# Optimization experiments

Measured on AMD Instinct MI355X. Metric: run time of the kernel, lower is better.

The kernel has to match this reference:

```python
import jax, jax.numpy as jnp
import numpy as np

LN_EPS = 1e-5
B, T, H = 32, 1024, 1024


def _layer_norm(v, g, b):
    m = v.mean(-1, keepdims=True)
    var = ((v - m) ** 2).mean(-1, keepdims=True)
    return (v - m) / jnp.sqrt(var + LN_EPS) * g + b


def setup_inputs() -> dict:
    key = jax.random.key(0)
    ks = jax.random.split(key, 10)
    s_t = 1.0 / np.sqrt(T)
    s_h = 1.0 / np.sqrt(H)
    return {
        "x": jax.random.normal(ks[0], (B, T, H), jnp.float32),
        # temporal MLP (square T x T, triangular-masked), torch Linear layout [out, in]
        "tw1": jax.random.uniform(ks[1], (T, T), jnp.float32, -s_t, s_t),
        "tb1": jax.random.uniform(ks[2], (T,), jnp.float32, -s_t, s_t),
        "tw2": jax.random.uniform(ks[3], (T, T), jnp.float32, -s_t, s_t),
        "tb2": jax.random.uniform(ks[4], (T,), jnp.float32, -s_t, s_t),
        # channel MLP (square H x H)
        "cw1": jax.random.uniform(ks[5], (H, H), jnp.float32, -s_h, s_h),
        "cb1": jax.random.uniform(ks[6], (H,), jnp.float32, -s_h, s_h),
        "cw2": jax.random.uniform(ks[7], (H, H), jnp.float32, -s_h, s_h),
        "cb2": jax.random.uniform(ks[8], (H,), jnp.float32, -s_h, s_h),
        # LayerNorm affine params
        "ln1_g": jnp.ones((H,), jnp.float32),
        "ln1_b": jnp.zeros((H,), jnp.float32),
        "ln2_g": jnp.ones((H,), jnp.float32),
        "ln2_b": jnp.zeros((H,), jnp.float32),
    }


def reference(x, tw1, tb1, tw2, tb2, cw1, cb1, cw2, cb2, ln1_g, ln1_b, ln2_g, ln2_b):
    t = tw1.shape[0]
    mask = jnp.tril(jnp.ones((t, t), x.dtype))  # diagonal=0: include self
    # temporal mixing: LN -> swap -> masked Linear -> GELU -> masked Linear -> swap
    y = _layer_norm(x, ln1_g, ln1_b)
    y = jnp.swapaxes(y, 1, 2)  # [B, H, T]
    y = y @ (mask * tw1).T + tb1
    y = jax.nn.gelu(y, approximate=False)
    y = y @ (mask * tw2).T + tb2
    y = jnp.swapaxes(y, 1, 2)  # [B, T, H]
    x = x + y
    # channel mixing: LN -> Linear -> GELU -> Linear
    y2 = _layer_norm(x, ln2_g, ln2_b)
    y2 = jax.nn.gelu(y2 @ cw1.T + cb1, approximate=False) @ cw2.T + cb2
    return x + y2
```

## Files before the change

kernel.cpp:

```cpp
#include <hip/hip_runtime.h>
#include <hip/hip_bf16.h>

#define BDIM 32
#define TDIM 1024
#define HDIM 1024
#define AS1 __attribute__((address_space(1)))
#define AS3 __attribute__((address_space(3)))

typedef __attribute__((ext_vector_type(8))) short short8;
typedef __attribute__((ext_vector_type(8))) unsigned short ushort8;
typedef __attribute__((ext_vector_type(4))) unsigned short u16x4;
typedef __attribute__((ext_vector_type(4))) float f32x4;

__device__ __forceinline__ float b2f(unsigned short h){ return __uint_as_float(((unsigned)h)<<16); }
__device__ __forceinline__ unsigned short f2b(float f){
  unsigned u = __float_as_uint(f);
  u += 0x7fffu + ((u>>16)&1u);
  return (unsigned short)(u>>16);
}
__device__ __forceinline__ float gelu_f(float v){ return 0.5f*v*(1.0f+erff(v*0.70710678118f)); }
__device__ __forceinline__ void stv(float* p, float v){ *p = v; }
__device__ __forceinline__ void stv(unsigned short* p, float v){ *p = f2b(v); }
__device__ __forceinline__ float ldr(float v){ return v; }
__device__ __forceinline__ float ldr(unsigned short v){ return b2f(v); }

__global__ void prep_weights(const float* __restrict__ w1, const float* __restrict__ w2,
                             const float* __restrict__ c1, const float* __restrict__ c2,
                             unsigned short* __restrict__ w1m, unsigned short* __restrict__ w2m,
                             unsigned short* __restrict__ c1b, unsigned short* __restrict__ c2b){
  int idx = blockIdx.x*blockDim.x + threadIdx.x;
  int e = idx*4;
  int i = e >> 10, j0 = e & 1023;
  f32x4 a = *(const f32x4*)(w1+e);
  f32x4 b = *(const f32x4*)(w2+e);
  f32x4 c = *(const f32x4*)(c1+e);
  f32x4 d = *(const f32x4*)(c2+e);
  u16x4 av, bv, cv, dv;
  #pragma unroll
  for (int q=0;q<4;++q){
    float am = (j0+q <= i) ? a[q] : 0.f;
    float bm = (j0+q <= i) ? b[q] : 0.f;
    av[q]=f2b(am); bv[q]=f2b(bm); cv[q]=f2b(c[q]); dv[q]=f2b(d[q]);
  }
  *(u16x4*)(w1m+e)=av; *(u16x4*)(w2m+e)=bv; *(u16x4*)(c1b+e)=cv; *(u16x4*)(c2b+e)=dv;
}

__global__ void ln_stats(const float* __restrict__ p, float* __restrict__ mean,
                         float* __restrict__ rstd){
  int wid = threadIdx.x>>6, lane = threadIdx.x&63;
  int row = blockIdx.x*4 + wid;
  const float* pr = p + (size_t)row*HDIM;
  float s=0.f, s2=0.f;
  #pragma unroll
  for (int it=0; it<4; ++it){
    f32x4 v = *(const f32x4*)(pr + it*256 + lane*4);
    #pragma unroll
    for (int c=0;c<4;++c){ s += v[c]; s2 += v[c]*v[c]; }
  }
  #pragma unroll
  for (int off=32; off>0; off>>=1){ s += __shfl_xor(s,off,64); s2 += __shfl_xor(s2,off,64); }
  if (lane==0){
    float m = s * (1.0f/HDIM);
    float var = s2 * (1.0f/HDIM) - m*m;
    mean[row]=m; rstd[row]=rsqrtf(var + 1e-5f);
  }
}

__global__ void ln_norm_transpose(const float* __restrict__ x, const float* __restrict__ mean,
                                  const float* __restrict__ rstd, const float* __restrict__ g,
                                  const float* __restrict__ bta, unsigned short* __restrict__ xnT){
  __shared__ float tile[64][65];
  int t0 = blockIdx.x*64, h0 = blockIdx.y*64, b = blockIdx.z;
  int tid = threadIdx.x;
  int rr = tid>>3, c8 = tid&7;
  size_t base = (size_t)b*TDIM*HDIM;
  #pragma unroll
  for (int p=0;p<2;++p){
    int r = rr + p*32;
    int trow = t0 + r;
    float m = mean[b*TDIM + trow], rs = rstd[b*TDIM + trow];
    f32x4 v0 = *(const f32x4*)(x + base + (size_t)trow*HDIM + h0 + c8*8);
    f32x4 v1 = *(const f32x4*)(x + base + (size_t)trow*HDIM + h0 + c8*8 + 4);
    #pragma unroll
    for (int c=0;c<4;++c){
      int h = c8*8+c;
      tile[r][h]   = (v0[c]-m)*rs*g[h0+h]   + bta[h0+h];
      tile[r][h+4] = (v1[c]-m)*rs*g[h0+h+4] + bta[h0+h+4];
    }
  }
  __syncthreads();
  #pragma unroll
  for (int p=0;p<2;++p){
    int hr = rr + p*32;
    ushort8 ov;
    #pragma unroll
    for (int c=0;c<8;++c) ov[c] = f2b(tile[c8*8+c][hr]);
    *(ushort8*)(xnT + base + (size_t)(h0+hr)*TDIM + t0 + c8*8) = ov;
  }
}

__global__ void ln_fused(const unsigned short* __restrict__ p, const float* __restrict__ g,
                         const float* __restrict__ bta, unsigned short* __restrict__ o){
  int wid = threadIdx.x>>6, lane = threadIdx.x&63;
  size_t row = (size_t)blockIdx.x*4 + wid;
  const unsigned short* pr = p + row*HDIM + lane*16;
  ushort8 v0 = *(const ushort8*)(pr);
  ushort8 v1 = *(const ushort8*)(pr+8);
  float f[16];
  float s=0.f, s2=0.f;
  #pragma unroll
  for (int c=0;c<8;++c){ f[c]=b2f(v0[c]); f[c+8]=b2f(v1[c]); }
  #pragma unroll
  for (int c=0;c<16;++c){ s += f[c]; s2 += f[c]*f[c]; }
  #pragma unroll
  for (int off=32; off>0; off>>=1){ s += __shfl_xor(s,off,64); s2 += __shfl_xor(s2,off,64); }
  float m = s * (1.0f/HDIM);
  float rs = rsqrtf(s2*(1.0f/HDIM) - m*m + 1e-5f);
  int h0 = lane*16;
  ushort8 o0, o1;
  #pragma unroll
  for (int c=0;c<8;++c){
    o0[c] = f2b((f[c]-m)*rs*g[h0+c] + bta[h0+c]);
    o1[c] = f2b((f[c+8]-m)*rs*g[h0+c+8] + bta[h0+c+8]);
  }
  *(ushort8*)(o + row*HDIM + h0) = o0;
  *(ushort8*)(o + row*HDIM + h0 + 8) = o1;
}

#define GATE(N) asm volatile("s_waitcnt vmcnt(" #N ")" ::: "memory")
#define BAR()   __builtin_amdgcn_s_barrier()

template<int MODE, typename CT, typename RT>
__global__ __launch_bounds__(512,1)
void gemmq(const unsigned short* __restrict__ act, const unsigned short* __restrict__ wgt,
           CT* __restrict__ C, const float* __restrict__ bias, const RT* __restrict__ resid){
  extern __shared__ char LDS[];
  const int bid = blockIdx.x;
  const int tile = (bid & 7)*64 + (bid >> 3);
  const int panel = tile >> 2;
  int inner = tile & 3;
  if constexpr (MODE==1 || MODE==2){ if (bid & 256) inner ^= 3; }
  const unsigned short *pa, *pb;
  size_t cbase; int rg0, cg0, kend;
  if constexpr (MODE==1){
    int b = panel>>2, mt = panel&3;
    pa = act + (size_t)b*1048576 + (size_t)mt*262144;
    pb = wgt + (size_t)inner*262144;
    kend = (inner+1)*256;
    cbase = (size_t)b*1048576; rg0 = mt*256; cg0 = inner*256;
  } else if constexpr (MODE==2){
    int b = panel>>2, nt = panel&3;
    pa = wgt + (size_t)inner*262144;
    pb = act + (size_t)b*1048576 + (size_t)nt*262144;
    kend = (inner+1)*256;
    cbase = (size_t)b*1048576; rg0 = inner*256; cg0 = nt*256;
  } else {
    pa = act + (size_t)panel*262144;
    pb = wgt + (size_t)inner*262144;
    kend = 1024;
    cbase = 0; rg0 = panel*256; cg0 = inner*256;
  }
  const int tid = threadIdx.x, lane = tid&63, wid = tid>>6;
  const int wrow = (wid>>2)*64;
  const int wcol = (wid&3)*32;
  const int l15 = lane&15, l4b = (lane>>4)<<4;
  f32x4 acc[8][4];
  #pragma unroll
  for (int i=0;i<8;++i)
    #pragma unroll
    for (int j=0;j<4;++j) acc[i][j] = (f32x4)(0.f);

  const int NT = kend>>6;

  auto STAGE = [&](int dstbuf, int half, int st){
    const unsigned short* src = (half<2) ? pa : pb;
    const int rbase = (half&1)<<7;
    char* dst = LDS + (dstbuf<<16) + (half<<14);
    const int k0 = st<<6;
    #pragma unroll
    for (int l=0;l<2;++l){
      int W = tid*16 + (l<<13);
      int r = W>>7;
      int cs = (W&127) ^ ((r&7)<<4);
      __builtin_amdgcn_global_load_lds(
        (const AS1 void*)(src + (size_t)(rbase+r)*1024 + k0 + (cs>>1)),
        (AS3 void*)(dst + W), 16, 0, 0);
    }
  };

  auto LDA = [&](int buf, int qa, int i, int s)->short8{
    int ra = wrow + i*16 + l15;
    int L = (ra<<7) + (((s<<6) + l4b) ^ ((ra&7)<<4));
    return *(const short8*)(LDS + (buf<<16) + (qa<<14) + L);
  };
  auto LDB = [&](int buf, int qb, int j, int s)->short8{
    int rb = wcol + j*16 + l15;
    int L = (rb<<7) + (((s<<6) + l4b) ^ ((rb&7)<<4));
    return *(const short8*)(LDS + (buf<<16) + ((2+qb)<<14) + L);
  };

  short8 aR[2][4], bR[2][2];

#define MFMAQ(qa,qb)                                                         \
  __builtin_amdgcn_s_setprio(1);                                             \
  _Pragma("unroll") for (int s=0;s<2;++s)                                    \
    _Pragma("unroll") for (int i=0;i<4;++i)                                  \
      _Pragma("unroll") for (int j=0;j<2;++j)                                \
        acc[(qa)*4+i][(qb)*2+j] = __builtin_amdgcn_mfma_f32_16x16x32_bf16(   \
            aR[s][i], bR[s][j], acc[(qa)*4+i][(qb)*2+j], 0,0,0);             \
  __builtin_amdgcn_s_setprio(0);

#define TILE_BODY(BUF, TT)                                                   \
  {                                                                          \
    const int nsrc = ((TT)+1 < NT) ? (TT)+1 : (TT);                          \
    STAGE(BUF^1, 0, nsrc); STAGE(BUF^1, 2, nsrc);                            \
    STAGE(BUF^1, 1, nsrc); STAGE(BUF^1, 3, nsrc);                            \
    GATE(8); BAR();                                                          \
    _Pragma("unroll") for (int s=0;s<2;++s){                                 \
      _Pragma("unroll") for (int i=0;i<4;++i) aR[s][i] = LDA(BUF,0,i,s);     \
      _Pragma("unroll") for (int j=0;j<2;++j) bR[s][j] = LDB(BUF,0,j,s);     \
    }                                                                        \
    MFMAQ(0,0)                                                               \
    _Pragma("unroll") for (int s=0;s<2;++s)                                  \
      _Pragma("unroll") for (int j=0;j<2;++j) bR[s][j] = LDB(BUF,1,j,s);     \
    MFMAQ(0,1)                                                               \
    _Pragma("unroll") for (int s=0;s<2;++s)                                  \
      _Pragma("unroll") for (int i=0;i<4;++i) aR[s][i] = LDA(BUF,1,i,s);     \
    MFMAQ(1,1)                                                               \
    _Pragma("unroll") for (int s=0;s<2;++s)                                  \
      _Pragma("unroll") for (int j=0;j<2;++j) bR[s][j] = LDB(BUF,0,j,s);     \
    MFMAQ(1,0)                                                               \
    BAR();                                                                   \
  }

  STAGE(0,0,0); STAGE(0,2,0); STAGE(0,1,0); STAGE(0,3,0);
  GATE(0); BAR();

  for (int t=0; t<NT; t+=2){
    TILE_BODY(0, t)
    TILE_BODY(1, t+1)
  }
#undef TILE_BODY
#undef MFMAQ

  GATE(0);

  #pragma unroll
  for (int I=0;I<8;++I){
    int rbase = rg0 + (I>>2)*128 + wrow + (I&3)*16 + ((lane>>4)<<2);
    #pragma unroll
    for (int J=0;J<4;++J){
      int cg = cg0 + (J>>1)*128 + wcol + (J&1)*16 + l15;
      float bn = (MODE!=2) ? bias[cg] : 0.f;
      #pragma unroll
      for (int r=0;r<4;++r){
        int rg = rbase + r;
        float v = acc[I][J][r];
        if (MODE==1 || MODE==3){ v += bn; v = gelu_f(v); }
        else if (MODE==2){ v += bias[rg]; v += ldr(resid[cbase + (size_t)rg*1024 + cg]); }
        else { v += bn; v += ldr(resid[cbase + (size_t)rg*1024 + cg]); }
        stv(&C[cbase + (size_t)rg*1024 + cg], v);
      }
    }
  }
}

extern "C" void kernel_launch(void* const* d_in, const int* in_sizes, int n_in,
                              void* d_out, int out_size, void* d_ws, size_t ws_size,
                              hipStream_t stream){
  const float* x    = (const float*)d_in[0];
  const float* tw1  = (const float*)d_in[1];
  const float* tb1  = (const float*)d_in[2];
  const float* tw2  = (const float*)d_in[3];
  const float* tb2  = (const float*)d_in[4];
  const float* cw1  = (const float*)d_in[5];
  const float* cb1  = (const float*)d_in[6];
  const float* cw2  = (const float*)d_in[7];
  const float* cb2  = (const float*)d_in[8];
  const float* g1   = (const float*)d_in[9];
  const float* bb1  = (const float*)d_in[10];
  const float* g2   = (const float*)d_in[11];
  const float* bb2  = (const float*)d_in[12];
  float* out = (float*)d_out;

  char* ws = (char*)d_ws;
  unsigned short* bufA = (unsigned short*)(ws);
  unsigned short* bufB = (unsigned short*)(ws + 67108864);
  unsigned short* xmid = (unsigned short*)(ws + 134217728);
  unsigned short* w1m  = (unsigned short*)(ws + 201326592);
  unsigned short* w2m  = (unsigned short*)(ws + 203423744);
  unsigned short* c1b  = (unsigned short*)(ws + 205520896);
  unsigned short* c2b  = (unsigned short*)(ws + 207618048);
  float* meanb = (float*)(ws + 209715200);
  float* rstdb = (float*)(ws + 209846272);

  prep_weights<<<1024,256,0,stream>>>(tw1,tw2,cw1,cw2,w1m,w2m,c1b,c2b);
  ln_stats<<<8192,256,0,stream>>>(x, meanb, rstdb);
  ln_norm_transpose<<<dim3(16,16,32),256,0,stream>>>(x, meanb, rstdb, g1, bb1, bufA);
  gemmq<1,unsigned short,float><<<512,512,131072,stream>>>(bufA, w1m, bufB, tb1, (const float*)nullptr);
  gemmq<2,unsigned short,float><<<512,512,131072,stream>>>(bufB, w2m, xmid, tb2, x);
  ln_fused<<<8192,256,0,stream>>>(xmid, g2, bb2, bufA);
  gemmq<3,unsigned short,unsigned short><<<512,512,131072,stream>>>(bufA, c1b, bufB, cb1, (const unsigned short*)nullptr);
  gemmq<4,float,unsigned short><<<512,512,131072,stream>>>(bufB, c2b, out, cb2, xmid);
}
```

Measured before the change: 501.4 us.

## Use 16 waves per GEMM block with 64x64 per-wave subtiles

The bf16 MFMA GEMM block grows from 512 to 1024 threads, so each of 16 waves computes a 64x64 sub-tile of the 256x256 output with 16 accumulators instead of 32. Each thread now issues one LDS-async load per staged half instead of two, and the quadrant-ordered MFMA schedule becomes a simple per-k-slice loop over B fragments. The aim is more waves to hide latency and lower register pressure per wave. The cost is more waves contending for barriers and LDS bandwidth, plus loss of the hand-tuned A/B fragment reuse ordering.

```diff
diff --git a/kernel.cpp b/kernel.cpp
--- a/kernel.cpp
+++ b/kernel.cpp
@@ -131,8 +131,8 @@
 #define BAR()   __builtin_amdgcn_s_barrier()
 
 template<int MODE, typename CT, typename RT>
-__global__ __launch_bounds__(512,1)
-void gemmq(const unsigned short* __restrict__ act, const unsigned short* __restrict__ wgt,
+__global__ __launch_bounds__(1024,1)
+void gemmw(const unsigned short* __restrict__ act, const unsigned short* __restrict__ wgt,
            CT* __restrict__ C, const float* __restrict__ bias, const RT* __restrict__ resid){
   extern __shared__ char LDS[];
   const int bid = blockIdx.x;
@@ -162,11 +162,14 @@
   }
   const int tid = threadIdx.x, lane = tid&63, wid = tid>>6;
   const int wrow = (wid>>2)*64;
-  const int wcol = (wid&3)*32;
+  const int wcol = (wid&3)*64;
   const int l15 = lane&15, l4b = (lane>>4)<<4;
-  f32x4 acc[8][4];
-  #pragma unroll
-  for (int i=0;i<8;++i)
+  const int abase = (wrow>>7)<<14;
+  const int bbase = 32768 + ((wcol>>7)<<14);
+  const int arow0 = wrow & 127, brow0 = wcol & 127;
+  f32x4 acc[4][4];
+  #pragma unroll
+  for (int i=0;i<4;++i)
     #pragma unroll
     for (int j=0;j<4;++j) acc[i][j] = (f32x4)(0.f);
 
@@ -176,64 +179,47 @@
     const unsigned short* src = (half<2) ? pa : pb;
     const int rbase = (half&1)<<7;
     char* dst = LDS + (dstbuf<<16) + (half<<14);
-    const int k0 = st<<6;
-    #pragma unroll
-    for (int l=0;l<2;++l){
-      int W = tid*16 + (l<<13);
-      int r = W>>7;
-      int cs = (W&127) ^ ((r&7)<<4);
-      __builtin_amdgcn_global_load_lds(
-        (const AS1 void*)(src + (size_t)(rbase+r)*1024 + k0 + (cs>>1)),
-        (AS3 void*)(dst + W), 16, 0, 0);
-    }
+    int W = tid*16;
+    int r = W>>7;
+    int cs = (W&127) ^ ((r&7)<<4);
+    __builtin_amdgcn_global_load_lds(
+      (const AS1 void*)(src + (size_t)(rbase+r)*1024 + (st<<6) + (cs>>1)),
+      (AS3 void*)(dst + W), 16, 0, 0);
   };
 
-  auto LDA = [&](int buf, int qa, int i, int s)->short8{
-    int ra = wrow + i*16 + l15;
+  auto LDA = [&](int buf, int i, int s)->short8{
+    int ra = arow0 + i*16 + l15;
     int L = (ra<<7) + (((s<<6) + l4b) ^ ((ra&7)<<4));
-    return *(const short8*)(LDS + (buf<<16) + (qa<<14) + L);
+    return *(const short8*)(LDS + (buf<<16) + abase + L);
   };
-  auto LDB = [&](int buf, int qb, int j, int s)->short8{
-    int rb = wcol + j*16 + l15;
+  auto LDB = [&](int buf, int j, int s)->short8{
+    int rb = brow0 + j*16 + l15;
     int L = (rb<<7) + (((s<<6) + l4b) ^ ((rb&7)<<4));
-    return *(const short8*)(LDS + (buf<<16) + ((2+qb)<<14) + L);
+    return *(const short8*)(LDS + (buf<<16) + bbase + L);
   };
-
-  short8 aR[2][4], bR[2][2];
-
-#define MFMAQ(qa,qb)                                                         \
-  __builtin_amdgcn_s_setprio(1);                                             \
-  _Pragma("unroll") for (int s=0;s<2;++s)                                    \
-    _Pragma("unroll") for (int i=0;i<4;++i)                                  \
-      _Pragma("unroll") for (int j=0;j<2;++j)                                \
-        acc[(qa)*4+i][(qb)*2+j] = __builtin_amdgcn_mfma_f32_16x16x32_bf16(   \
-            aR[s][i], bR[s][j], acc[(qa)*4+i][(qb)*2+j], 0,0,0);             \
-  __builtin_amdgcn_s_setprio(0);
 
 #define TILE_BODY(BUF, TT)                                                   \
   {                                                                          \
     const int nsrc = ((TT)+1 < NT) ? (TT)+1 : (TT);                          \
-    STAGE(BUF^1, 0, nsrc); STAGE(BUF^1, 2, nsrc);                            \
-    STAGE(BUF^1, 1, nsrc); STAGE(BUF^1, 3, nsrc);                            \
-    GATE(8); BAR();                                                          \
+    STAGE(BUF^1, 0, nsrc); STAGE(BUF^1, 1, nsrc);                            \
+    STAGE(BUF^1, 2, nsrc); STAGE(BUF^1, 3, nsrc);                            \
+    GATE(4); BAR();                                                          \
     _Pragma("unroll") for (int s=0;s<2;++s){                                 \
-      _Pragma("unroll") for (int i=0;i<4;++i) aR[s][i] = LDA(BUF,0,i,s);     \
-      _Pragma("unroll") for (int j=0;j<2;++j) bR[s][j] = LDB(BUF,0,j,s);     \
+      short8 aR[4];                                                          \
+      _Pragma("unroll") for (int i=0;i<4;++i) aR[i] = LDA(BUF,i,s);          \
+      _Pragma("unroll") for (int j=0;j<4;++j){                               \
+        short8 bR = LDB(BUF,j,s);                                            \
+        __builtin_amdgcn_s_setprio(1);                                       \
+        _Pragma("unroll") for (int i=0;i<4;++i)                              \
+          acc[i][j] = __builtin_amdgcn_mfma_f32_16x16x32_bf16(               \
+              aR[i], bR, acc[i][j], 0,0,0);                                  \
+        __builtin_amdgcn_s_setprio(0);                                       \
+      }                                                                      \
     }                                                                        \
-    MFMAQ(0,0)                                                               \
-    _Pragma("unroll") for (int s=0;s<2;++s)                                  \
-      _Pragma("unroll") for (int j=0;j<2;++j) bR[s][j] = LDB(BUF,1,j,s);     \
-    MFMAQ(0,1)                                                               \
-    _Pragma("unroll") for (int s=0;s<2;++s)                                  \
-      _Pragma("unroll") for (int i=0;i<4;++i) aR[s][i] = LDA(BUF,1,i,s);     \
-    MFMAQ(1,1)                                                               \
-    _Pragma("unroll") for (int s=0;s<2;++s)                                  \
-      _Pragma("unroll") for (int j=0;j<2;++j) bR[s][j] = LDB(BUF,0,j,s);     \
-    MFMAQ(1,0)                                                               \
     BAR();                                                                   \
   }
 
-  STAGE(0,0,0); STAGE(0,2,0); STAGE(0,1,0); STAGE(0,3,0);
+  STAGE(0,0,0); STAGE(0,1,0); STAGE(0,2,0); STAGE(0,3,0);
   GATE(0); BAR();
 
   for (int t=0; t<NT; t+=2){
@@ -241,21 +227,20 @@
     TILE_BODY(1, t+1)
   }
 #undef TILE_BODY
-#undef MFMAQ
 
   GATE(0);
 
   #pragma unroll
-  for (int I=0;I<8;++I){
-    int rbase = rg0 + (I>>2)*128 + wrow + (I&3)*16 + ((lane>>4)<<2);
-    #pragma unroll
-    for (int J=0;J<4;++J){
-      int cg = cg0 + (J>>1)*128 + wcol + (J&1)*16 + l15;
+  for (int i=0;i<4;++i){
+    int rbase = rg0 + wrow + i*16 + ((lane>>4)<<2);
+    #pragma unroll
+    for (int j=0;j<4;++j){
+      int cg = cg0 + wcol + j*16 + l15;
       float bn = (MODE!=2) ? bias[cg] : 0.f;
       #pragma unroll
       for (int r=0;r<4;++r){
         int rg = rbase + r;
-        float v = acc[I][J][r];
+        float v = acc[i][j][r];
         if (MODE==1 || MODE==3){ v += bn; v = gelu_f(v); }
         else if (MODE==2){ v += bias[rg]; v += ldr(resid[cbase + (size_t)rg*1024 + cg]); }
         else { v += bn; v += ldr(resid[cbase + (size_t)rg*1024 + cg]); }
@@ -297,9 +282,9 @@
   prep_weights<<<1024,256,0,stream>>>(tw1,tw2,cw1,cw2,w1m,w2m,c1b,c2b);
   ln_stats<<<8192,256,0,stream>>>(x, meanb, rstdb);
   ln_norm_transpose<<<dim3(16,16,32),256,0,stream>>>(x, meanb, rstdb, g1, bb1, bufA);
-  gemmq<1,unsigned short,float><<<512,512,131072,stream>>>(bufA, w1m, bufB, tb1, (const float*)nullptr);
-  gemmq<2,unsigned short,float><<<512,512,131072,stream>>>(bufB, w2m, xmid, tb2, x);
+  gemmw<1,unsigned short,float><<<512,1024,131072,stream>>>(bufA, w1m, bufB, tb1, (const float*)nullptr);
+  gemmw<2,unsigned short,float><<<512,1024,131072,stream>>>(bufB, w2m, xmid, tb2, x);
   ln_fused<<<8192,256,0,stream>>>(xmid, g2, bb2, bufA);
-  gemmq<3,unsigned short,unsigned short><<<512,512,131072,stream>>>(bufA, c1b, bufB, cb1, (const unsigned short*)nullptr);
-  gemmq<4,float,unsigned short><<<512,512,131072,stream>>>(bufB, c2b, out, cb2, xmid);
-}
+  gemmw<3,unsigned short,unsigned short><<<512,1024,131072,stream>>>(bufA, c1b, bufB, cb1, (const unsigned short*)nullptr);
+  gemmw<4,float,unsigned short><<<512,1024,131072,stream>>>(bufB, c2b, out, cb2, xmid);
+}
```

After: 483.6 us. 1.04x faster.
